# Optimization experiments

Measured on AMD Instinct MI355X. Metric: run time of the kernel, lower is better.

## Reference

```python
import jax, jax.numpy as jnp
import numpy as np

DEPTH = 2
D_MODEL = 768
D_STATE = 64
EXPAND = 2
D_CONV = 4
D_INNER = EXPAND * D_MODEL          # 1536
DT_RANK = (D_MODEL + 15) // 16      # 48
BATCH, SEQ = 4, 2048


def setup_inputs() -> dict:
    key = jax.random.key(0)
    ks = jax.random.split(key, 8)
    s = 0.02  # small init scale for stability
    return {
        "x": jax.random.normal(ks[0], (BATCH, SEQ, D_MODEL), jnp.float32),
        # per-layer params stacked along leading DEPTH axis
        "in_proj_w": jax.random.normal(ks[1], (DEPTH, 2 * D_INNER, D_MODEL), jnp.float32) * s,
        "conv_w": jax.random.normal(ks[2], (DEPTH, D_INNER, D_CONV), jnp.float32) * s,
        "conv_b": jnp.zeros((DEPTH, D_INNER), jnp.float32),
        "x_proj_w": jax.random.normal(ks[3], (DEPTH, DT_RANK + 2 * D_STATE, D_INNER), jnp.float32) * s,
        "dt_proj_w": jax.random.normal(ks[4], (DEPTH, D_INNER, DT_RANK), jnp.float32) * s,
        "dt_proj_b": jax.random.normal(ks[5], (DEPTH, D_INNER), jnp.float32) * s,
        # S4D-real init: A = -[1..N] per channel -> A_log = log(arange)
        "A_log": jnp.tile(jnp.log(jnp.arange(1, D_STATE + 1, dtype=jnp.float32))[None, None, :],
                          (DEPTH, D_INNER, 1)),
        "D_skip": jnp.ones((DEPTH, D_INNER), jnp.float32),
        "out_proj_w": jax.random.normal(ks[6], (DEPTH, D_MODEL, D_INNER), jnp.float32) * s,
    }


def _causal_conv1d(x, w, b):
    # depthwise causal conv: x [B,L,d], w [d,K], b [d]
    L = x.shape[1]
    xp = jnp.pad(x, ((0, 0), (D_CONV - 1, 0), (0, 0)))
    y = b
    for k in range(D_CONV):
        y = y + xp[:, k:k + L, :] * w[:, k]
    return y


def _selective_scan(u, dt, A, Bm, Cm):
    # u, dt: [B,L,d]; A: [d,N]; Bm, Cm: [B,L,N]
    def step(h, inp):
        dt_t, B_t, C_t, u_t = inp  # [B,d],[B,N],[B,N],[B,d]
        dA = jnp.exp(dt_t[..., None] * A)                         # [B,d,N]
        h = dA * h + dt_t[..., None] * B_t[:, None, :] * u_t[..., None]
        y_t = jnp.einsum('bdn,bn->bd', h, C_t)
        return h, y_t

    h0 = jnp.zeros((u.shape[0], u.shape[2], A.shape[1]), u.dtype)
    xs = (jnp.swapaxes(dt, 0, 1), jnp.swapaxes(Bm, 0, 1),
          jnp.swapaxes(Cm, 0, 1), jnp.swapaxes(u, 0, 1))
    _, ys = jax.lax.scan(step, h0, xs)  # ys [L,B,d]
    return jnp.swapaxes(ys, 0, 1)


def _mamba_layer(x, Wi, cw, cb, Wx, Wdt, bdt, A_log, Dp, Wo):
    xz = x @ Wi.T                                  # [B,L,2*d_inner]
    xpart, z = jnp.split(xz, 2, axis=-1)
    xpart = jax.nn.silu(_causal_conv1d(xpart, cw, cb))
    xdbl = xpart @ Wx.T                            # [B,L,dt_rank+2N]
    dt_in, Bm, Cm = jnp.split(xdbl, [DT_RANK, DT_RANK + D_STATE], axis=-1)
    dt = jax.nn.softplus(dt_in @ Wdt.T + bdt)      # [B,L,d_inner]
    A = -jnp.exp(A_log)                            # [d_inner, N]
    y = _selective_scan(xpart, dt, A, Bm, Cm) + Dp * xpart
    y = y * jax.nn.silu(z)
    return y @ Wo.T                                # [B,L,d_model]


def reference(x, in_proj_w, conv_w, conv_b, x_proj_w, dt_proj_w, dt_proj_b,
              A_log, D_skip, out_proj_w):
    for i in range(DEPTH):
        x = _mamba_layer(x, in_proj_w[i], conv_w[i], conv_b[i], x_proj_w[i],
                         dt_proj_w[i], dt_proj_b[i], A_log[i], D_skip[i],
                         out_proj_w[i])
    return x
```

## Files before the change

### kernel.cpp

```cpp
#include <hip/hip_runtime.h>
#include <hip/hip_bf16.h>
#include <math.h>

#define DEPTH   2
#define DM      768
#define DS      64
#define DC      4
#define DI      1536
#define DTR     48
#define BATCH   4
#define SEQ     2048
#define MROWS   (BATCH*SEQ)
#define XDC     (DTR + 2*DS)
#define NC      8
#define TCH     (SEQ/NC)
#define LOG2E   1.44269504088896f

typedef __attribute__((ext_vector_type(8))) short bf16x8;
typedef __attribute__((ext_vector_type(4))) float f32x4;
typedef unsigned short ushort_t;
#define GAS __attribute__((address_space(1)))
#define LAS __attribute__((address_space(3)))

__device__ __forceinline__ float silu_fast(float x) {
    return x / (1.f + __expf(-x));
}
__device__ __forceinline__ float softplus_acc(float x) {
    return x > 20.f ? x : log1pf(expf(x));
}

__device__ __forceinline__ ushort_t bf16_hi(float f) {
    unsigned u = __float_as_uint(f);
    unsigned hr = u + 0x7FFF + ((u >> 16) & 1);
    return (ushort_t)(hr >> 16);
}

__global__ __launch_bounds__(256) void quant_bf16(
    const float* __restrict__ in, ushort_t* __restrict__ hi)
{
    const size_t i = ((size_t)blockIdx.x * 256 + threadIdx.x) * 4;
    const float4 v = *(const float4*)(in + i);
    ushort4 h;
    h.x = bf16_hi(v.x); h.y = bf16_hi(v.y);
    h.z = bf16_hi(v.z); h.w = bf16_hi(v.w);
    *(ushort4*)(hi + i) = h;
}

__global__ __launch_bounds__(256, 2) void gemm_mfma(
    const ushort_t* __restrict__ A, const ushort_t* __restrict__ W,
    float* __restrict__ C, int N, int K, int ldA, int ldW,
    ushort_t* __restrict__ Chi, float4* __restrict__ bc4out, int mode)
{
    __shared__ ushort_t lds[2][128 * 32];
    const int tid  = threadIdx.x;
    const int wave = tid >> 6, lane = tid & 63;

    int bx = blockIdx.x, by = blockIdx.y;
    {
        const int X   = gridDim.x;
        const int fid = by * X + bx;
        const int xcd = fid & 7;
        const int j   = fid >> 3;
        const int jX  = j / X;
        by = xcd * (gridDim.y >> 3) + jX;
        bx = j - jX * X;
    }
    const int bm0 = by * 128, bn0 = bx * 128;
    const int wm = (wave >> 1) * 64, wn = (wave & 1) * 64;

    const int srow = lane >> 2;
    const int skq  = (lane & 3) * 8;

    f32x4 acc[4][4];
#pragma unroll
    for (int i = 0; i < 4; i++)
#pragma unroll
        for (int j = 0; j < 4; j++) acc[i][j] = (f32x4){0.f, 0.f, 0.f, 0.f};

    const int lm  = lane & 15;
    const int kg8 = (lane >> 4) * 8;

    for (int k0 = 0; k0 < K; k0 += 32) {
#pragma unroll
        for (int j = 0; j < 4; j++) {
            const int ldid = wave * 4 + j;
            const int buf  = ldid >> 3;
            const int slot = ldid & 7;
            const ushort_t* gsrc = buf ? W : A;
            const int ldg = buf ? ldW : ldA;
            const int rb  = buf ? bn0 : bm0;
            const ushort_t* ga = gsrc + (size_t)(rb + slot * 16 + srow) * ldg + k0 + skq;
            __builtin_amdgcn_global_load_lds(
                (const GAS unsigned*)ga, (LAS unsigned*)&lds[buf][slot * 512], 16, 0, 0);
        }
        __syncthreads();

        bf16x8 ah[4], bh[4];
#pragma unroll
        for (int i = 0; i < 4; i++) {
            const int ar = (wm + i * 16 + lm) * 32 + kg8;
            ah[i] = *(const bf16x8*)&lds[0][ar];
            const int br = (wn + i * 16 + lm) * 32 + kg8;
            bh[i] = *(const bf16x8*)&lds[1][br];
        }
#pragma unroll
        for (int mi = 0; mi < 4; mi++)
#pragma unroll
            for (int ni = 0; ni < 4; ni++)
                acc[mi][ni] = __builtin_amdgcn_mfma_f32_16x16x32_bf16(
                    ah[mi], bh[ni], acc[mi][ni], 0, 0, 0);
        __syncthreads();
    }

#pragma unroll
    for (int mi = 0; mi < 4; mi++)
#pragma unroll
        for (int ni = 0; ni < 4; ni++) {
            const int rowb = bm0 + wm + mi * 16 + (lane >> 4) * 4;
            const int colg = bn0 + wn + ni * 16 + lm;
            if (mode == 1) {
#pragma unroll
                for (int r = 0; r < 4; r++)
                    Chi[(size_t)(rowb + r) * N + colg] = bf16_hi(acc[mi][ni][r]);
            } else if (mode == 2) {
                if (colg >= DTR && colg < DTR + 2 * DS) {
                    const f32x4 a = acc[mi][ni];
                    bc4out[(size_t)(rowb >> 2) * 128 + (colg - DTR)] =
                        make_float4(a[0], a[1], a[2], a[3]);
                } else if (colg < DTR) {
#pragma unroll
                    for (int r = 0; r < 4; r++)
                        C[(size_t)(rowb + r) * N + colg] = acc[mi][ni][r];
                }
            } else {
#pragma unroll
                for (int r = 0; r < 4; r++)
                    if (colg < N)
                        C[(size_t)(rowb + r) * N + colg] = acc[mi][ni][r];
            }
        }
}

__global__ __launch_bounds__(256, 2) void gemm_dt_T(
    const float* __restrict__ Wdt, const float* __restrict__ xdbl,
    const float* __restrict__ bias, float* __restrict__ dtT)
{
    __shared__ float As[8][132];
    __shared__ float Bs[8][132];
    const int tid = threadIdx.x;
    const int bd0 = blockIdx.y * 128;
    const int bt0 = blockIdx.x * 128;
    const int b   = blockIdx.z;
    const int tx = tid & 15;
    const int ty = tid >> 4;
    const int lrow = tid >> 1;
    const int lk4  = (tid & 1) * 4;

    float acc[8][8];
#pragma unroll
    for (int i = 0; i < 8; i++)
#pragma unroll
        for (int j = 0; j < 8; j++) acc[i][j] = 0.f;

    for (int k0 = 0; k0 < DTR; k0 += 8) {
        const float4 av = *(const float4*)(Wdt + (size_t)(bd0 + lrow) * DTR + k0 + lk4);
        const float4 wv = *(const float4*)(xdbl + ((size_t)b * SEQ + bt0 + lrow) * XDC + k0 + lk4);
        __syncthreads();
        As[lk4 + 0][lrow] = av.x; As[lk4 + 1][lrow] = av.y;
        As[lk4 + 2][lrow] = av.z; As[lk4 + 3][lrow] = av.w;
        Bs[lk4 + 0][lrow] = wv.x; Bs[lk4 + 1][lrow] = wv.y;
        Bs[lk4 + 2][lrow] = wv.z; Bs[lk4 + 3][lrow] = wv.w;
        __syncthreads();
#pragma unroll
        for (int kk = 0; kk < 8; kk++) {
            const float4 a0 = *(const float4*)&As[kk][ty * 8];
            const float4 a1 = *(const float4*)&As[kk][ty * 8 + 4];
            const float4 b0 = *(const float4*)&Bs[kk][tx * 8];
            const float4 b1 = *(const float4*)&Bs[kk][tx * 8 + 4];
            const float ar[8] = {a0.x, a0.y, a0.z, a0.w, a1.x, a1.y, a1.z, a1.w};
            const float br[8] = {b0.x, b0.y, b0.z, b0.w, b1.x, b1.y, b1.z, b1.w};
#pragma unroll
            for (int i = 0; i < 8; i++)
#pragma unroll
                for (int j = 0; j < 8; j++)
                    acc[i][j] = fmaf(ar[i], br[j], acc[i][j]);
        }
    }

#pragma unroll
    for (int i = 0; i < 8; i++) {
        const int d = bd0 + ty * 8 + i;
        const float bb = bias[d];
#pragma unroll
        for (int j4 = 0; j4 < 8; j4 += 4) {
            float4 v = make_float4(acc[i][j4], acc[i][j4 + 1], acc[i][j4 + 2], acc[i][j4 + 3]);
            v.x = softplus_acc(v.x + bb);
            v.y = softplus_acc(v.y + bb);
            v.z = softplus_acc(v.z + bb);
            v.w = softplus_acc(v.w + bb);
            *(float4*)(dtT + ((size_t)b * DI + d) * SEQ + bt0 + tx * 8 + j4) = v;
        }
    }
}

__global__ __launch_bounds__(256) void conv_silu_T2(
    const float* __restrict__ xz, const float* __restrict__ cw,
    const float* __restrict__ cb, float* __restrict__ uT,
    ushort_t* __restrict__ uh)
{
    __shared__ float tin[67][65];
    __shared__ float ttr[64][65];
    const int tid = threadIdx.x;
    const int d0 = blockIdx.x * 64, t0 = blockIdx.y * 64, b = blockIdx.z;
    const int cl = tid & 63, q = tid >> 6;

    for (int r = q; r < 67; r += 4) {
        const int t = t0 - 3 + r;
        float v = 0.f;
        if (t >= 0) v = xz[((size_t)b * SEQ + t) * (2 * DI) + d0 + cl];
        tin[r][cl] = v;
    }
    __syncthreads();

    const float4 w = ((const float4*)cw)[d0 + cl];
    const float bb = cb[d0 + cl];
#pragma unroll
    for (int i = 0; i < 16; i++) {
        const int t = q * 16 + i;
        float a = bb;
        a = fmaf(tin[t + 0][cl], w.x, a);
        a = fmaf(tin[t + 1][cl], w.y, a);
        a = fmaf(tin[t + 2][cl], w.z, a);
        a = fmaf(tin[t + 3][cl], w.w, a);
        a = silu_fast(a);
        ttr[cl][t] = a;
        const size_t row = (size_t)b * SEQ + t0 + t;
        uh[row * DI + d0 + cl] = bf16_hi(a);
    }
    __syncthreads();
#pragma unroll
    for (int i = 0; i < 16; i++) {
        const int d = q * 16 + i;
        uT[((size_t)b * DI + d0 + d) * SEQ + t0 + cl] = ttr[d][cl];
    }
}


#define LOAD4S(DT, UU, BB_, CC_, TB)                                   \
    _Pragma("unroll")                                                  \
    for (int g = 0; g < 4; g++) {                                      \
        DT[g]  = *(const float4*)(dtp + (TB) + 4 * g);                 \
        UU[g]  = *(const float4*)(up + (TB) + 4 * g);                  \
        BB_[g] = Bp[(size_t)((TB) / 4 + g) * 128];                     \
        CC_[g] = Cp[(size_t)((TB) / 4 + g) * 128];                     \
    }

#define P3_BLOCK(DT, UU, BB_, CC_, TBASE)                                                          \
    {                                                                                              \
        float p[16];                                                                               \
        _Pragma("unroll")                                                                          \
        for (int g = 0; g < 4; g++) {                                                              \
            h = fmaf(__builtin_amdgcn_exp2f(DT[g].x * An), h, (DT[g].x * UU[g].x) * BB_[g].x); p[4*g+0] = h * CC_[g].x; \
            h = fmaf(__builtin_amdgcn_exp2f(DT[g].y * An), h, (DT[g].y * UU[g].y) * BB_[g].y); p[4*g+1] = h * CC_[g].y; \
            h = fmaf(__builtin_amdgcn_exp2f(DT[g].z * An), h, (DT[g].z * UU[g].z) * BB_[g].z); p[4*g+2] = h * CC_[g].z; \
            h = fmaf(__builtin_amdgcn_exp2f(DT[g].w * An), h, (DT[g].w * UU[g].w) * BB_[g].w); p[4*g+3] = h * CC_[g].w; \
        }                                                                                          \
        _Pragma("unroll")                                                                          \
        for (int i = 0; i < 16; i++) slab[i * 65 + lane] = p[i];                                   \
        float s = 0.f;                                                                             \
        _Pragma("unroll")                                                                          \
        for (int j = 0; j < 16; j++) s += slab[tt * 65 + seg * 16 + j];                            \
        s += __shfl_xor(s, 16, 64);                                                                \
        s += __shfl_xor(s, 32, 64);                                                                \
        if (lane < 16) sp[(TBASE) + tt] = s;                                                       \
    }

__global__ __launch_bounds__(256, 2) void scan_tail(
    const float* __restrict__ dtT, const float* __restrict__ uT,
    const float4* __restrict__ bc4, const float* __restrict__ A_log,
    float* __restrict__ hend)
{
    const int wid  = __builtin_amdgcn_readfirstlane(
                        (int)((blockIdx.x * 256 + threadIdx.x) >> 6));
    const int lane = threadIdx.x & 63;
    const int c  = wid & (NC - 1);
    const int bd = wid >> 3;
    const int b  = bd / DI;
    const int d  = bd - b * DI;

    const float An = -expf(A_log[d * DS + lane]) * LOG2E;
    const float* dtp = dtT + (size_t)bd * SEQ + c * TCH;
    const float* up  = uT  + (size_t)bd * SEQ + c * TCH;
    const float4* Bp = bc4 + ((size_t)b * (SEQ / 4) + c * (TCH / 4)) * 128 + lane;

    float h = 0.f, r = 0.f;
    for (int tb = TCH - 16; tb >= 0; tb -= 16) {
        float4 dt4[4], u4[4], B4[4];
#pragma unroll
        for (int g = 0; g < 4; g++) {
            dt4[g] = *(const float4*)(dtp + tb + 4 * g);
            u4[g]  = *(const float4*)(up  + tb + 4 * g);
            B4[g]  = Bp[(size_t)(tb / 4 + g) * 128];
        }
#pragma unroll
        for (int g = 3; g >= 0; g--) {
            h = fmaf(__builtin_amdgcn_exp2f(An * r), (dt4[g].w * u4[g].w) * B4[g].w, h); r += dt4[g].w;
            h = fmaf(__builtin_amdgcn_exp2f(An * r), (dt4[g].z * u4[g].z) * B4[g].z, h); r += dt4[g].z;
            h = fmaf(__builtin_amdgcn_exp2f(An * r), (dt4[g].y * u4[g].y) * B4[g].y, h); r += dt4[g].y;
            h = fmaf(__builtin_amdgcn_exp2f(An * r), (dt4[g].x * u4[g].x) * B4[g].x, h); r += dt4[g].x;
        }
        if (__all(An * r < -30.f)) break;
    }
    hend[(size_t)wid * DS + lane] = h;
}

__global__ __launch_bounds__(256) void scan_phase2(
    const float* __restrict__ dtT, const float* __restrict__ A_log,
    const float* __restrict__ hend, float* __restrict__ h0out)
{
    const int bd   = (blockIdx.x * 256 + threadIdx.x) >> 6;
    const int lane = threadIdx.x & 63;
    const int d    = bd % DI;

    const float* dtp = dtT + (size_t)bd * SEQ + lane * 32;
    float s = 0.f;
#pragma unroll
    for (int g = 0; g < 8; g++) {
        const float4 v = *(const float4*)(dtp + 4 * g);
        s += (v.x + v.y) + (v.z + v.w);
    }
    s += __shfl_xor(s, 1, 64);
    s += __shfl_xor(s, 2, 64);
    s += __shfl_xor(s, 4, 64);

    const float An = -expf(A_log[d * DS + lane]) * LOG2E;
    float h = 0.f;
#pragma unroll
    for (int c = 0; c < NC; c++) {
        const float sdt = __shfl(s, 8 * c, 64);
        const size_t off = ((size_t)bd * NC + c) * DS + lane;
        h0out[off] = h;
        h = fmaf(__builtin_amdgcn_exp2f(An * sdt), h, hend[off]);
    }
}

__global__ __launch_bounds__(256, 2) void scan_phase3(
    const float* __restrict__ dtT, const float* __restrict__ uT,
    const float4* __restrict__ bc4, const float* __restrict__ A_log,
    const float* __restrict__ hin, float* __restrict__ sX)
{
    __shared__ float red[4][16 * 65];
    const int wid  = __builtin_amdgcn_readfirstlane(
                        (int)((blockIdx.x * 256 + threadIdx.x) >> 6));
    const int lane = threadIdx.x & 63;
    const int c  = wid & (NC - 1);
    const int bd = wid >> 3;
    const int b  = bd / DI;
    const int d  = bd - b * DI;

    const float An = -expf(A_log[d * DS + lane]) * LOG2E;
    const float* dtp = dtT + (size_t)bd * SEQ + c * TCH;
    const float* up  = uT  + (size_t)bd * SEQ + c * TCH;
    const float4* Bp = bc4 + ((size_t)b * (SEQ / 4) + c * (TCH / 4)) * 128 + lane;
    const float4* Cp = Bp + 64;
    const size_t L0 = (size_t)bd * SEQ + c * TCH;
    float* sp = sX + (L0 / 1536) * 3072 + (L0 % 1536);
    float* slab = &red[threadIdx.x >> 6][0];
    const int tt = lane & 15, seg = lane >> 4;

    float4 dA4[4], uA4[4], BA4[4], CA4[4], dB4[4], uB4[4], BB4[4], CB4[4];
    LOAD4S(dA4, uA4, BA4, CA4, 0);

    float h = hin[(size_t)wid * DS + lane];
    for (int tb = 0; tb < TCH; tb += 32) {
        LOAD4S(dB4, uB4, BB4, CB4, tb + 16);
        P3_BLOCK(dA4, uA4, BA4, CA4, tb);
        LOAD4S(dA4, uA4, BA4, CA4, tb + 32);
        P3_BLOCK(dB4, uB4, BB4, CB4, tb + 16);
    }
}

__global__ __launch_bounds__(256) void gate_split_T(
    const float* __restrict__ xz, const float* __restrict__ uT,
    const float* __restrict__ Dskip, ushort_t* __restrict__ yh)
{
    __shared__ float zt[64][65];
    __shared__ float yt[64][65];
    const int tid = threadIdx.x;
    const int d0 = blockIdx.x * 64, t0 = blockIdx.y * 64, b = blockIdx.z;
    const int cl = tid & 63, q = tid >> 6;
#pragma unroll
    for (int i = 0; i < 16; i++) {
        const int r = q * 16 + i;
        zt[r][cl] = xz[((size_t)b * SEQ + t0 + r) * (2 * DI) + DI + d0 + cl];
    }
    __syncthreads();
#pragma unroll
    for (int i = 0; i < 16; i++) {
        const int dd = q * 16 + i;
        const size_t Lrow = ((size_t)b * DI + d0 + dd) * SEQ + t0;
        const float s = xz[(Lrow / 1536) * 3072 + (Lrow % 1536) + cl];
        const float u = uT[Lrow + cl];
        const float Dd = Dskip[d0 + dd];
        yt[dd][cl] = (s + Dd * u) * silu_fast(zt[cl][dd]);
    }
    __syncthreads();
#pragma unroll
    for (int i = 0; i < 16; i++) {
        const int t = q * 16 + i;
        const size_t row = (size_t)b * SEQ + t0 + t;
        yh[row * DI + d0 + cl] = bf16_hi(yt[cl][t]);
    }
}

extern "C" void kernel_launch(void* const* d_in, const int* in_sizes, int n_in,
                              void* d_out, int out_size, void* d_ws, size_t ws_size,
                              hipStream_t stream) {
    (void)in_sizes; (void)n_in; (void)out_size; (void)ws_size;
    const float* x    = (const float*)d_in[0];
    const float* Wi   = (const float*)d_in[1];
    const float* cw   = (const float*)d_in[2];
    const float* cb   = (const float*)d_in[3];
    const float* Wx   = (const float*)d_in[4];
    const float* Wdt  = (const float*)d_in[5];
    const float* bdt  = (const float*)d_in[6];
    const float* Alog = (const float*)d_in[7];
    const float* Dsk  = (const float*)d_in[8];
    const float* Wo   = (const float*)d_in[9];
    float* out = (float*)d_out;

    float* xz    = (float*)d_ws;
    float* uT    = xz    + (size_t)MROWS * (2 * DI);
    float* dtT   = uT    + (size_t)MROWS * DI;
    float* xdbl  = dtT   + (size_t)MROWS * DI;
    float* bcT   = xdbl  + (size_t)MROWS * XDC;
    float* xnext = bcT   + (size_t)BATCH * 128 * SEQ;
    float* hend  = xnext;
    float* h0buf = xnext + (size_t)BATCH * DI * NC * DS;

    ushort_t* sh  = (ushort_t*)uT;
    ushort_t* wih = (ushort_t*)(dtT + (size_t)MROWS * DM);
    ushort_t* uh  = (ushort_t*)dtT;
    ushort_t* wxh = (ushort_t*)xnext;
    ushort_t* woh = (ushort_t*)xdbl;
    ushort_t* yh  = (ushort_t*)xnext;

    for (int i = 0; i < DEPTH; i++) {
        const float* Wi_l   = Wi   + (size_t)i * 2 * DI * DM;
        const float* cw_l   = cw   + (size_t)i * DI * DC;
        const float* cb_l   = cb   + (size_t)i * DI;
        const float* Wx_l   = Wx   + (size_t)i * XDC * DI;
        const float* Wdt_l  = Wdt  + (size_t)i * DI * DTR;
        const float* bdt_l  = bdt  + (size_t)i * DI;
        const float* Alog_l = Alog + (size_t)i * DI * DS;
        const float* Dsk_l  = Dsk  + (size_t)i * DI;
        const float* Wo_l   = Wo   + (size_t)i * DM * DI;

        if (i == 0)
            quant_bf16<<<(size_t)MROWS * DM / 1024, 256, 0, stream>>>(x, sh);
        quant_bf16<<<(size_t)2 * DI * DM / 1024, 256, 0, stream>>>(Wi_l, wih);
        gemm_mfma<<<dim3(2 * DI / 128, MROWS / 128), 256, 0, stream>>>(
            sh, wih, xz, 2 * DI, DM, DM, DM, nullptr, nullptr, 0);
        conv_silu_T2<<<dim3(DI / 64, SEQ / 64, BATCH), 256, 0, stream>>>(
            xz, cw_l, cb_l, uT, uh);
        quant_bf16<<<(size_t)XDC * DI / 1024, 256, 0, stream>>>(Wx_l, wxh);
        gemm_mfma<<<dim3((XDC + 127) / 128, MROWS / 128), 256, 0, stream>>>(
            uh, wxh, xdbl, XDC, DI, DI, DI, nullptr, (float4*)bcT, 2);
        gemm_dt_T<<<dim3(SEQ / 128, DI / 128, BATCH), 256, 0, stream>>>(
            Wdt_l, xdbl, bdt_l, dtT);
        scan_tail<<<(BATCH * DI * NC) / 4, 256, 0, stream>>>(
            dtT, uT, (const float4*)bcT, Alog_l, hend);
        scan_phase2<<<(BATCH * DI) / 4, 256, 0, stream>>>(
            dtT, Alog_l, hend, h0buf);
        scan_phase3<<<(BATCH * DI * NC) / 4, 256, 0, stream>>>(
            dtT, uT, (const float4*)bcT, Alog_l, h0buf, xz);
        gate_split_T<<<dim3(DI / 64, SEQ / 64, BATCH), 256, 0, stream>>>(
            xz, uT, Dsk_l, yh);
        quant_bf16<<<(size_t)DM * DI / 1024, 256, 0, stream>>>(Wo_l, woh);
        if (i == DEPTH - 1)
            gemm_mfma<<<dim3(DM / 128, MROWS / 128), 256, 0, stream>>>(
                yh, woh, out, DM, DI, DI, DI, nullptr, nullptr, 0);
        else
            gemm_mfma<<<dim3(DM / 128, MROWS / 128), 256, 0, stream>>>(
                yh, woh, xz , DM, DI, DI, DI, sh, nullptr, 1);
    }
}
```

Measured before the change: 1.209 ms.

## Process two channels per wave in scan phase3 with cross-lane reduction

Each wave in scan_phase3 now handles two (batch, channel) pairs at once using float2 packed math. This halves the grid and reuses each B/C load across both channels. The LDS slab reduction over the 64 state lanes is replaced by a register-only tree of permlane swaps and DPP row sums, which removes the shared memory traffic and its bank pressure. In exchange, register pressure per wave is higher and there are fewer waves to hide latency.

```diff
diff --git a/kernel.cpp b/kernel.cpp
--- a/kernel.cpp
+++ b/kernel.cpp
@@ -18,6 +18,8 @@
 
 typedef __attribute__((ext_vector_type(8))) short bf16x8;
 typedef __attribute__((ext_vector_type(4))) float f32x4;
+typedef __attribute__((ext_vector_type(2))) float f32x2;
+typedef __attribute__((ext_vector_type(2))) unsigned int uint2v;
 typedef unsigned short ushort_t;
 #define GAS __attribute__((address_space(1)))
 #define LAS __attribute__((address_space(3)))
@@ -33,6 +35,55 @@
     unsigned u = __float_as_uint(f);
     unsigned hr = u + 0x7FFF + ((u >> 16) & 1);
     return (ushort_t)(hr >> 16);
+}
+
+__device__ __forceinline__ f32x2 merge_x32_2(f32x2 a, f32x2 b) {
+#if __has_builtin(__builtin_amdgcn_permlane32_swap)
+    const uint2v rx = __builtin_amdgcn_permlane32_swap(
+        __float_as_uint(a.x), __float_as_uint(b.x), false, false);
+    const uint2v ry = __builtin_amdgcn_permlane32_swap(
+        __float_as_uint(a.y), __float_as_uint(b.y), false, false);
+    const f32x2 s0 = {__uint_as_float(rx[0]), __uint_as_float(ry[0])};
+    const f32x2 s1 = {__uint_as_float(rx[1]), __uint_as_float(ry[1])};
+    return s0 + s1;
+#else
+    const f32x2 sa = {a.x + __shfl_xor(a.x, 32, 64), a.y + __shfl_xor(a.y, 32, 64)};
+    const f32x2 sb = {b.x + __shfl_xor(b.x, 32, 64), b.y + __shfl_xor(b.y, 32, 64)};
+    return (threadIdx.x & 32) ? sb : sa;
+#endif
+}
+
+__device__ __forceinline__ f32x2 merge_x16_2(f32x2 a, f32x2 b) {
+#if __has_builtin(__builtin_amdgcn_permlane16_swap)
+    const uint2v rx = __builtin_amdgcn_permlane16_swap(
+        __float_as_uint(a.x), __float_as_uint(b.x), false, false);
+    const uint2v ry = __builtin_amdgcn_permlane16_swap(
+        __float_as_uint(a.y), __float_as_uint(b.y), false, false);
+    const f32x2 s0 = {__uint_as_float(rx[0]), __uint_as_float(ry[0])};
+    const f32x2 s1 = {__uint_as_float(rx[1]), __uint_as_float(ry[1])};
+    return s0 + s1;
+#else
+    const f32x2 sa = {a.x + __shfl_xor(a.x, 16, 64), a.y + __shfl_xor(a.y, 16, 64)};
+    const f32x2 sb = {b.x + __shfl_xor(b.x, 16, 64), b.y + __shfl_xor(b.y, 16, 64)};
+    return (threadIdx.x & 16) ? sb : sa;
+#endif
+}
+
+template <int CTRL>
+__device__ __forceinline__ f32x2 dpp_add2(f32x2 x) {
+    const int tx = __builtin_amdgcn_update_dpp(
+        0, __float_as_int(x.x), CTRL, 0xF, 0xF, true);
+    const int ty = __builtin_amdgcn_update_dpp(
+        0, __float_as_int(x.y), CTRL, 0xF, 0xF, true);
+    const f32x2 t = {__int_as_float(tx), __int_as_float(ty)};
+    return x + t;
+}
+__device__ __forceinline__ f32x2 rowsum16_2(f32x2 x) {
+    x = dpp_add2<0x128>(x);
+    x = dpp_add2<0x124>(x);
+    x = dpp_add2<0x122>(x);
+    x = dpp_add2<0x121>(x);
+    return x;
 }
 
 __global__ __launch_bounds__(256) void quant_bf16(
@@ -246,35 +297,6 @@
 }
 
 
-#define LOAD4S(DT, UU, BB_, CC_, TB)                                   \
-    _Pragma("unroll")                                                  \
-    for (int g = 0; g < 4; g++) {                                      \
-        DT[g]  = *(const float4*)(dtp + (TB) + 4 * g);                 \
-        UU[g]  = *(const float4*)(up + (TB) + 4 * g);                  \
-        BB_[g] = Bp[(size_t)((TB) / 4 + g) * 128];                     \
-        CC_[g] = Cp[(size_t)((TB) / 4 + g) * 128];                     \
-    }
-
-#define P3_BLOCK(DT, UU, BB_, CC_, TBASE)                                                          \
-    {                                                                                              \
-        float p[16];                                                                               \
-        _Pragma("unroll")                                                                          \
-        for (int g = 0; g < 4; g++) {                                                              \
-            h = fmaf(__builtin_amdgcn_exp2f(DT[g].x * An), h, (DT[g].x * UU[g].x) * BB_[g].x); p[4*g+0] = h * CC_[g].x; \
-            h = fmaf(__builtin_amdgcn_exp2f(DT[g].y * An), h, (DT[g].y * UU[g].y) * BB_[g].y); p[4*g+1] = h * CC_[g].y; \
-            h = fmaf(__builtin_amdgcn_exp2f(DT[g].z * An), h, (DT[g].z * UU[g].z) * BB_[g].z); p[4*g+2] = h * CC_[g].z; \
-            h = fmaf(__builtin_amdgcn_exp2f(DT[g].w * An), h, (DT[g].w * UU[g].w) * BB_[g].w); p[4*g+3] = h * CC_[g].w; \
-        }                                                                                          \
-        _Pragma("unroll")                                                                          \
-        for (int i = 0; i < 16; i++) slab[i * 65 + lane] = p[i];                                   \
-        float s = 0.f;                                                                             \
-        _Pragma("unroll")                                                                          \
-        for (int j = 0; j < 16; j++) s += slab[tt * 65 + seg * 16 + j];                            \
-        s += __shfl_xor(s, 16, 64);                                                                \
-        s += __shfl_xor(s, 32, 64);                                                                \
-        if (lane < 16) sp[(TBASE) + tt] = s;                                                       \
-    }
-
 __global__ __launch_bounds__(256, 2) void scan_tail(
     const float* __restrict__ dtT, const float* __restrict__ uT,
     const float4* __restrict__ bc4, const float* __restrict__ A_log,
@@ -344,39 +366,100 @@
     }
 }
 
+
+#define LOAD6(D0, D1, U0, U1, BB_, CC_, TB)                            \
+    _Pragma("unroll")                                                  \
+    for (int g = 0; g < 4; g++) {                                      \
+        D0[g]  = *(const float4*)(dtp0 + (TB) + 4 * g);                \
+        D1[g]  = *(const float4*)(dtp1 + (TB) + 4 * g);                \
+        U0[g]  = *(const float4*)(up0 + (TB) + 4 * g);                 \
+        U1[g]  = *(const float4*)(up1 + (TB) + 4 * g);                 \
+        BB_[g] = Bp[(size_t)((TB) / 4 + g) * 128];                     \
+        CC_[g] = Cp[(size_t)((TB) / 4 + g) * 128];                     \
+    }
+
+#define P3_STEP(E, G, D0, D1, U0, U1, BB_, CC_, LF)                    \
+    {                                                                  \
+        const f32x2 dte = {D0[G].E, D1[G].E};                          \
+        const f32x2 ue  = {U0[G].E, U1[G].E};                          \
+        f32x2 w2 = dte * An2;                                          \
+        const f32x2 ee = {__builtin_amdgcn_exp2f(w2.x),                \
+                          __builtin_amdgcn_exp2f(w2.y)};               \
+        const f32x2 p2 = (dte * ue) * BB_[G].E;                        \
+        h2 = ee * h2 + p2;                                             \
+        LF = h2 * CC_[G].E;                                            \
+    }
+
+#define P3_BLOCK(D0, D1, U0, U1, BB_, CC_, TBASE)                      \
+    {                                                                  \
+        f32x2 m[8];                                                    \
+        _Pragma("unroll")                                              \
+        for (int g = 0; g < 4; g++) {                                  \
+            f32x2 lf0, lf1, lf2, lf3;                                  \
+            P3_STEP(x, g, D0, D1, U0, U1, BB_, CC_, lf0)               \
+            P3_STEP(y, g, D0, D1, U0, U1, BB_, CC_, lf1)               \
+            P3_STEP(z, g, D0, D1, U0, U1, BB_, CC_, lf2)               \
+            P3_STEP(w, g, D0, D1, U0, U1, BB_, CC_, lf3)               \
+            m[2 * g]     = merge_x32_2(lf0, lf1);                      \
+            m[2 * g + 1] = merge_x32_2(lf2, lf3);                      \
+        }                                                              \
+        const f32x2 q0 = rowsum16_2(merge_x16_2(m[0], m[1]));          \
+        const f32x2 q1 = rowsum16_2(merge_x16_2(m[2], m[3]));          \
+        const f32x2 q2 = rowsum16_2(merge_x16_2(m[4], m[5]));          \
+        const f32x2 q3 = rowsum16_2(merge_x16_2(m[6], m[7]));          \
+        const f32x2 v = (lane & 2) ? ((lane & 1) ? q3 : q2)            \
+                                   : ((lane & 1) ? q1 : q0);           \
+        if ((lane & 15) < 4) {                                         \
+            sp0[(TBASE) + wtt] = v.x;                                  \
+            sp1[(TBASE) + wtt] = v.y;                                  \
+        }                                                              \
+    }
+
 __global__ __launch_bounds__(256, 2) void scan_phase3(
     const float* __restrict__ dtT, const float* __restrict__ uT,
     const float4* __restrict__ bc4, const float* __restrict__ A_log,
     const float* __restrict__ hin, float* __restrict__ sX)
 {
-    __shared__ float red[4][16 * 65];
+    const int tid  = threadIdx.x;
     const int wid  = __builtin_amdgcn_readfirstlane(
-                        (int)((blockIdx.x * 256 + threadIdx.x) >> 6));
-    const int lane = threadIdx.x & 63;
-    const int c  = wid & (NC - 1);
-    const int bd = wid >> 3;
-    const int b  = bd / DI;
-    const int d  = bd - b * DI;
-
-    const float An = -expf(A_log[d * DS + lane]) * LOG2E;
-    const float* dtp = dtT + (size_t)bd * SEQ + c * TCH;
-    const float* up  = uT  + (size_t)bd * SEQ + c * TCH;
+                        (int)((blockIdx.x * 256 + tid) >> 6));
+    const int lane = tid & 63;
+    const int c   = wid & (NC - 1);
+    const int bdq = wid >> 3;
+    const int bd0 = bdq * 2;
+    const int b   = bd0 / DI;
+    const int d0  = bd0 - b * DI;
+
+    const f32x2 An2 = {-expf(A_log[(size_t)d0 * DS + lane]) * LOG2E,
+                       -expf(A_log[(size_t)(d0 + 1) * DS + lane]) * LOG2E};
+
+    const float* dtp0 = dtT + (size_t)bd0 * SEQ + c * TCH;
+    const float* dtp1 = dtp0 + SEQ;
+    const float* up0  = uT  + (size_t)bd0 * SEQ + c * TCH;
+    const float* up1  = up0 + SEQ;
     const float4* Bp = bc4 + ((size_t)b * (SEQ / 4) + c * (TCH / 4)) * 128 + lane;
     const float4* Cp = Bp + 64;
-    const size_t L0 = (size_t)bd * SEQ + c * TCH;
-    float* sp = sX + (L0 / 1536) * 3072 + (L0 % 1536);
-    float* slab = &red[threadIdx.x >> 6][0];
-    const int tt = lane & 15, seg = lane >> 4;
-
-    float4 dA4[4], uA4[4], BA4[4], CA4[4], dB4[4], uB4[4], BB4[4], CB4[4];
-    LOAD4S(dA4, uA4, BA4, CA4, 0);
-
-    float h = hin[(size_t)wid * DS + lane];
+
+    const size_t L0 = (size_t)bd0 * SEQ + c * TCH;
+    const size_t L1 = L0 + SEQ;
+    float* sp0 = sX + (L0 / 1536) * 3072 + (L0 % 1536);
+    float* sp1 = sX + (L1 / 1536) * 3072 + (L1 % 1536);
+
+    const int wr  = lane >> 4;
+    const int wtt = 4 * (lane & 3) + (((wr & 1) << 1) | (wr >> 1));
+
+    f32x2 h2 = {hin[((size_t)bd0 * NC + c) * DS + lane],
+                hin[((size_t)(bd0 + 1) * NC + c) * DS + lane]};
+
+    float4 dA0[4], dA1[4], uA0[4], uA1[4], BA4[4], CA4[4];
+    float4 dB0[4], dB1[4], uB0[4], uB1[4], BB4[4], CB4[4];
+    LOAD6(dA0, dA1, uA0, uA1, BA4, CA4, 0);
+
     for (int tb = 0; tb < TCH; tb += 32) {
-        LOAD4S(dB4, uB4, BB4, CB4, tb + 16);
-        P3_BLOCK(dA4, uA4, BA4, CA4, tb);
-        LOAD4S(dA4, uA4, BA4, CA4, tb + 32);
-        P3_BLOCK(dB4, uB4, BB4, CB4, tb + 16);
+        LOAD6(dB0, dB1, uB0, uB1, BB4, CB4, tb + 16);
+        P3_BLOCK(dA0, dA1, uA0, uA1, BA4, CA4, tb);
+        LOAD6(dA0, dA1, uA0, uA1, BA4, CA4, tb + 32);
+        P3_BLOCK(dB0, dB1, uB0, uB1, BB4, CB4, tb + 16);
     }
 }
 
@@ -472,7 +555,7 @@
             dtT, uT, (const float4*)bcT, Alog_l, hend);
         scan_phase2<<<(BATCH * DI) / 4, 256, 0, stream>>>(
             dtT, Alog_l, hend, h0buf);
-        scan_phase3<<<(BATCH * DI * NC) / 4, 256, 0, stream>>>(
+        scan_phase3<<<(BATCH * DI * NC) / 8, 256, 0, stream>>>(
             dtT, uT, (const float4*)bcT, Alog_l, h0buf, xz);
         gate_split_T<<<dim3(DI / 64, SEQ / 64, BATCH), 256, 0, stream>>>(
             xz, uT, Dsk_l, yh);
```

Measured after the change: 1.115 ms. -7.8%, faster.
